# Kernel tuning notes

Measured on AMD Instinct MI355X. Metric: run time of the kernel, lower is better.

Reference implementation:

```python
import jax, jax.numpy as jnp
import numpy as np

NUM_HEADS = 16

def setup_inputs() -> dict:
    key = jax.random.key(0)
    k0, k1, k2, k3 = jax.random.split(key, 4)
    B, N, Nl, Nr, D = 16, 257, 514, 512, 1024
    gather_idx = jax.random.randint(k0, (B, N), 0, B * Nl + Nr, dtype=jnp.int64 if jax.config.jax_enable_x64 else jnp.int32)
    lhs_states = jax.random.normal(k1, (4, B, Nl, D), dtype=jnp.float32)
    rhs_states = jax.random.normal(k2, (4, 1, Nr, D), dtype=jnp.float32)
    Wo = jax.random.normal(k3, (D, D), dtype=jnp.float32) * 0.02
    bo = jnp.zeros((D,), dtype=jnp.float32)
    return {"gather_idx": gather_idx, "lhs_states": lhs_states, "rhs_states": rhs_states, "Wo": Wo, "bo": bo}


def _gather_stacked_batched_states(gather_idx, lhs_states, rhs_states):
    # lhs_states: [4, B, Nl, D] cache; rhs_states: [4, 1, Nr, D]
    # torch builds batched_states [4, 1, B*Nl+Nr, D] then gathers with [4, B, N, D] idx
    S, B, Nl, D = lhs_states.shape
    Nr = rhs_states.shape[2]
    batched = jnp.concatenate(
        [lhs_states.reshape(S, B * Nl, D), rhs_states.reshape(S, Nr, D)], axis=1
    )  # [4, B*Nl+Nr, D]
    N = gather_idx.shape[1]
    gathered = jnp.take(batched, gather_idx.reshape(-1), axis=1)  # [4, B*N, D]
    return gathered.reshape(S, B, N, D)


def reference(gather_idx, lhs_states, rhs_states, Wo, bo):
    # Gather hidden/q/k/v states from the expanded cache buffer (token reuse dispatch)
    gathered = _gather_stacked_batched_states(gather_idx, lhs_states, rhs_states)
    hidden, q, k, v = gathered[0], gathered[1], gathered[2], gathered[3]
    B, N, D = hidden.shape
    H = NUM_HEADS
    hd = D // H
    scale = hd ** -0.5
    # _shape: [B, N, D] -> [B, H, N, hd]; query scaled before bmm as in torch
    qh = (q * scale).reshape(B, N, H, hd).transpose(0, 2, 1, 3)
    kh = k.reshape(B, N, H, hd).transpose(0, 2, 1, 3)
    vh = v.reshape(B, N, H, hd).transpose(0, 2, 1, 3)
    attn_weights = jax.nn.softmax(jnp.einsum('bhqd,bhkd->bhqk', qh, kh), axis=-1)
    attn_out = jnp.einsum('bhqk,bhkd->bhqd', attn_weights, vh)  # [B, H, N, hd]
    attn_out = attn_out.transpose(0, 2, 1, 3).reshape(B, N, D)
    attn_out = attn_out @ Wo.T + bo  # out_proj (torch Linear)
    return hidden + attn_out  # residual
```

## Files before the change

### kernel.cpp

```cpp
#include <hip/hip_runtime.h>
#include <hip/hip_bf16.h>

typedef __attribute__((ext_vector_type(8))) short bf16x8;
typedef __attribute__((ext_vector_type(4))) float f32x4;
typedef unsigned short u16;
typedef unsigned int u32;

#define LHS_STRIDE 8421376
#define RHS_STRIDE 524288
#define TBL_SPLIT  8224
#define AN 257
#define KSD 68
#define VSD 260

__device__ __forceinline__ const float* tbl_row(int s, int g,
    const float* __restrict__ lhs, const float* __restrict__ rhs) {
  if (g < TBL_SPLIT) return lhs + (size_t)s * LHS_STRIDE + (size_t)g * 1024;
  return rhs + (size_t)s * RHS_STRIDE + (size_t)(g - TBL_SPLIT) * 1024;
}

__device__ __forceinline__ u16 f2b(float x) {
  union { __hip_bfloat16 b; u16 u; } c;
  c.b = __float2bfloat16(x);
  return c.u;
}

__device__ __forceinline__ u32 pk2(float a, float b) {
  return (u32)f2b(a) | ((u32)f2b(b) << 16);
}

__device__ __forceinline__ bf16x8 mk8(ushort4 a, ushort4 b) {
  bf16x8 r;
  r[0] = (short)a.x; r[1] = (short)a.y; r[2] = (short)a.z; r[3] = (short)a.w;
  r[4] = (short)b.x; r[5] = (short)b.y; r[6] = (short)b.z; r[7] = (short)b.w;
  return r;
}

__device__ __forceinline__ void gload16(const u16* g, u16* l) {
  __builtin_amdgcn_global_load_lds((const __attribute__((address_space(1))) void*)g,
                                   (__attribute__((address_space(3))) void*)l,
                                   16, 0, 0);
}

struct __align__(16) AttnSmem {
  u16 K[272 * KSD];
  u16 VT[64 * VSD];
};

__global__ __launch_bounds__(512, 2) void attn_kernel(
    const int* __restrict__ gidx, const float* __restrict__ lhs,
    const float* __restrict__ rhs, u16* __restrict__ attn_out,
    const float* __restrict__ Wo, u16* __restrict__ wo_bf) {
  __shared__ AttnSmem sm;
  const int bh = blockIdx.x, b = bh >> 4, h = bh & 15;
  const int t = threadIdx.x, wave = t >> 6, lane = t & 63;
  const int lg = lane >> 4, lr = lane & 15;
  const int* gi = gidx + b * AN;

  const int sr = t >> 4, c4v = (t & 15) * 4;
  float4 kreg[9], vreg[9];
#pragma unroll
  for (int p = 0; p < 9; ++p) {
    int r = p * 32 + sr;
    int rc = (r < AN) ? r : 0;
    int g = gi[rc];
    kreg[p] = *(const float4*)(tbl_row(2, g, lhs, rhs) + h * 64 + c4v);
    vreg[p] = *(const float4*)(tbl_row(3, g, lhs, rhs) + h * 64 + c4v);
  }

  const int ntile = (wave == 0) ? 3 : 2;
  const int rts[3] = {wave, wave + 8, 16};
  bf16x8 qa[3][2];
#pragma unroll
  for (int ti = 0; ti < 3; ++ti) {
    if (ti < ntile) {
      int qrow = rts[ti] * 16 + lr; if (qrow > 256) qrow = 256;
      int g = gi[qrow];
      const float* qp = tbl_row(1, g, lhs, rhs) + h * 64 + lg * 8;
#pragma unroll
      for (int kf = 0; kf < 2; ++kf) {
        float4 v0 = *(const float4*)(qp + kf * 32);
        float4 v1 = *(const float4*)(qp + kf * 32 + 4);
        bf16x8 a;
        a[0] = (short)f2b(0.125f * v0.x); a[1] = (short)f2b(0.125f * v0.y);
        a[2] = (short)f2b(0.125f * v0.z); a[3] = (short)f2b(0.125f * v0.w);
        a[4] = (short)f2b(0.125f * v1.x); a[5] = (short)f2b(0.125f * v1.y);
        a[6] = (short)f2b(0.125f * v1.z); a[7] = (short)f2b(0.125f * v1.w);
        qa[ti][kf] = a;
      }
    }
  }

  {
    const float4* src = (const float4*)Wo;
    ushort4* dst = (ushort4*)wo_bf;
    int i0 = bh * 1024 + t * 2;
#pragma unroll
    for (int u = 0; u < 2; ++u) {
      float4 v = src[i0 + u];
      dst[i0 + u] = make_ushort4(f2b(v.x), f2b(v.y), f2b(v.z), f2b(v.w));
    }
  }

#pragma unroll
  for (int p = 0; p < 9; ++p) {
    int r = p * 32 + sr;
    if (r < AN) {
      *(ushort4*)&sm.K[r * KSD + c4v] =
          make_ushort4(f2b(kreg[p].x), f2b(kreg[p].y), f2b(kreg[p].z), f2b(kreg[p].w));
      sm.VT[(c4v + 0) * VSD + r] = f2b(vreg[p].x);
      sm.VT[(c4v + 1) * VSD + r] = f2b(vreg[p].y);
      sm.VT[(c4v + 2) * VSD + r] = f2b(vreg[p].z);
      sm.VT[(c4v + 3) * VSD + r] = f2b(vreg[p].w);
    }
  }
  __syncthreads();

  const int srcE = lr + ((lane & 16) << 1);
  const int srcO = srcE + 16;
  const bool useE = (lg < 2);

  for (int ti = 0; ti < ntile; ++ti) {
    const int r0 = rts[ti] * 16;

    f32x4 s[17];
#pragma unroll
    for (int nf = 0; nf < 17; ++nf) {
      const u16* kp = &sm.K[(nf * 16 + lr) * KSD + lg * 8];
      ushort4 x0 = *(const ushort4*)kp;
      ushort4 x1 = *(const ushort4*)(kp + 4);
      ushort4 y0 = *(const ushort4*)(kp + 32);
      ushort4 y1 = *(const ushort4*)(kp + 36);
      f32x4 acc = {0.f, 0.f, 0.f, 0.f};
      acc = __builtin_amdgcn_mfma_f32_16x16x32_bf16(mk8(x0, x1), qa[ti][0], acc, 0, 0, 0);
      acc = __builtin_amdgcn_mfma_f32_16x16x32_bf16(mk8(y0, y1), qa[ti][1], acc, 0, 0, 0);
      s[nf] = acc;
    }
    s[16][1] = -1e30f; s[16][2] = -1e30f; s[16][3] = -1e30f;
    if (lg != 0) s[16][0] = -1e30f;

    float m = -1e30f;
#pragma unroll
    for (int nf = 0; nf < 17; ++nf)
      m = fmaxf(m, fmaxf(fmaxf(s[nf][0], s[nf][1]), fmaxf(s[nf][2], s[nf][3])));
    m = fmaxf(m, __shfl_xor(m, 16));
    m = fmaxf(m, __shfl_xor(m, 32));
    float sum = 0.f;
#pragma unroll
    for (int nf = 0; nf < 17; ++nf) {
#pragma unroll
      for (int r = 0; r < 4; ++r) {
        float w = __expf(s[nf][r] - m);
        s[nf][r] = w;
        sum += w;
      }
    }
    sum += __shfl_xor(sum, 16);
    sum += __shfl_xor(sum, 32);
    const float inv = 1.0f / sum;

    f32x4 zero = {0.f, 0.f, 0.f, 0.f};
    f32x4 o[4] = {zero, zero, zero, zero};
#pragma unroll
    for (int ks = 0; ks < 8; ++ks) {
      u32 e0 = pk2(s[2 * ks][0] * inv, s[2 * ks][1] * inv);
      u32 e1 = pk2(s[2 * ks][2] * inv, s[2 * ks][3] * inv);
      u32 f0 = pk2(s[2 * ks + 1][0] * inv, s[2 * ks + 1][1] * inv);
      u32 f1 = pk2(s[2 * ks + 1][2] * inv, s[2 * ks + 1][3] * inv);
      u32 A0 = (u32)__shfl((int)e0, srcE), A1 = (u32)__shfl((int)e1, srcE);
      u32 A2 = (u32)__shfl((int)e0, srcO), A3 = (u32)__shfl((int)e1, srcO);
      u32 B0 = (u32)__shfl((int)f0, srcE), B1 = (u32)__shfl((int)f1, srcE);
      u32 B2 = (u32)__shfl((int)f0, srcO), B3 = (u32)__shfl((int)f1, srcO);
      union { u32 w[4]; bf16x8 v; } pa;
      pa.w[0] = useE ? A0 : B0; pa.w[1] = useE ? A1 : B1;
      pa.w[2] = useE ? A2 : B2; pa.w[3] = useE ? A3 : B3;
#pragma unroll
      for (int nd = 0; nd < 4; ++nd) {
        const u16* vp = &sm.VT[(nd * 16 + lr) * VSD + ks * 32 + lg * 8];
        bf16x8 vb = mk8(*(const ushort4*)vp, *(const ushort4*)(vp + 4));
        o[nd] = __builtin_amdgcn_mfma_f32_16x16x32_bf16(pa.v, vb, o[nd], 0, 0, 0);
      }
    }
    {
      union { u32 w[4]; bf16x8 v; } pa;
      pa.w[0] = pk2(s[16][0] * inv, 0.f);
      pa.w[1] = 0; pa.w[2] = 0; pa.w[3] = 0;
#pragma unroll
      for (int nd = 0; nd < 4; ++nd) {
        union { u32 w[4]; bf16x8 v; } vb;
        vb.w[0] = (lg == 0) ? (u32)sm.VT[(nd * 16 + lr) * VSD + 256] : 0u;
        vb.w[1] = 0; vb.w[2] = 0; vb.w[3] = 0;
        o[nd] = __builtin_amdgcn_mfma_f32_16x16x32_bf16(pa.v, vb.v, o[nd], 0, 0, 0);
      }
    }

#pragma unroll
    for (int nd = 0; nd < 4; ++nd)
#pragma unroll
      for (int reg = 0; reg < 4; ++reg) {
        int row = r0 + lg * 4 + reg;
        if (row < AN)
          attn_out[(size_t)(b * AN + row) * 1024 + h * 64 + nd * 16 + lr] =
              f2b(o[nd][reg]);
      }
  }
}

__global__ __launch_bounds__(256, 1) void gemm_kernel(
    const u16* __restrict__ A, const u16* __restrict__ Bw,
    const float* __restrict__ bo, const int* __restrict__ gidx,
    const float* __restrict__ lhs, const float* __restrict__ rhs,
    float* __restrict__ out) {
  __shared__ __align__(16) u16 As[2][128 * 32];
  __shared__ __align__(16) u16 Bs[2][128 * 32];
  const int t = threadIdx.x, wave = t >> 6, lane = t & 63;
  const int lg = lane >> 4, lr = lane & 15;
  const int mt = blockIdx.x >> 3, nt = blockIdx.x & 7;
  const int m0 = mt * 128, n0 = nt * 128;
  const int wm = wave >> 1, wn = wave & 1;

  f32x4 zero = {0.f, 0.f, 0.f, 0.f};
  f32x4 acc[4][4];
#pragma unroll
  for (int i = 0; i < 4; ++i)
#pragma unroll
    for (int j = 0; j < 4; ++j) acc[i][j] = zero;

  const int srow = lane >> 2;
  const int scol = (((lane & 3) ^ ((lane >> 3) & 3))) * 8;
  const int ss = (lg ^ ((lr >> 1) & 3)) * 8;

#define STAGE(buf, kt)                                                          \
  {                                                                             \
    const int k0 = (kt) * 32;                                                   \
    _Pragma("unroll")                                                           \
    for (int i = 0; i < 2; ++i) {                                               \
      int row = wave * 32 + i * 16 + srow;                                      \
      int arow = m0 + row; if (arow > 4111) arow = 4111;                        \
      gload16(A + (size_t)arow * 1024 + k0 + scol, &As[buf][wave * 1024 + i * 512]); \
      gload16(Bw + (size_t)(n0 + row) * 1024 + k0 + scol, &Bs[buf][wave * 1024 + i * 512]); \
    }                                                                           \
  }

  STAGE(0, 0)
  __syncthreads();
  int cur = 0;
  for (int kt = 0; kt < 32; ++kt) {
    if (kt < 31) STAGE(cur ^ 1, kt + 1)
    bf16x8 af[4], bfr[4];
#pragma unroll
    for (int i = 0; i < 4; ++i) {
      af[i]  = *(const bf16x8*)&As[cur][(wm * 64 + i * 16 + lr) * 32 + ss];
      bfr[i] = *(const bf16x8*)&Bs[cur][(wn * 64 + i * 16 + lr) * 32 + ss];
    }
#pragma unroll
    for (int i = 0; i < 4; ++i)
#pragma unroll
      for (int j = 0; j < 4; ++j)
        acc[i][j] = __builtin_amdgcn_mfma_f32_16x16x32_bf16(af[i], bfr[j], acc[i][j], 0, 0, 0);
    __syncthreads();
    cur ^= 1;
  }
#undef STAGE

#pragma unroll
  for (int i = 0; i < 4; ++i)
#pragma unroll
    for (int j = 0; j < 4; ++j)
#pragma unroll
      for (int reg = 0; reg < 4; ++reg) {
        int row = m0 + wm * 64 + i * 16 + lg * 4 + reg;
        int col = n0 + wn * 64 + j * 16 + lr;
        if (row < 4112) {
          int g = gidx[row];
          out[(size_t)row * 1024 + col] =
              tbl_row(0, g, lhs, rhs)[col] + bo[col] + acc[i][j][reg];
        }
      }
}

extern "C" void kernel_launch(void* const* d_in, const int* in_sizes, int n_in,
                              void* d_out, int out_size, void* d_ws, size_t ws_size,
                              hipStream_t stream) {
  const int*   gidx = (const int*)d_in[0];
  const float* lhs  = (const float*)d_in[1];
  const float* rhs  = (const float*)d_in[2];
  const float* Wo   = (const float*)d_in[3];
  const float* bo   = (const float*)d_in[4];
  float* out = (float*)d_out;

  u16* attn_ws = (u16*)d_ws;
  u16* wo_bf   = attn_ws + (size_t)4112 * 1024;

  attn_kernel<<<256, 512, 0, stream>>>(gidx, lhs, rhs, attn_ws, Wo, wo_bf);
  gemm_kernel<<<264, 256, 0, stream>>>(attn_ws, wo_bf, bo, gidx, lhs, rhs, out);
}
```

Baseline: 302.2 us.

## Split gather and bf16 conversion into a separate full-row kernel before attention

Adds a gather_cvt kernel that fetches each gathered Q/K/V row and each Wo row as a full contiguous 4 KB fp32 row, converts it to bf16 and writes it to workspace. The attention kernel then reads compact bf16 tiles instead of doing scattered 256-byte fp32 gathers. The K smem stride also changes, and the GEMM block index is remapped so that concurrently scheduled blocks share A/B tiles differently. The cost is an extra launch and a round-trip of bf16 Q/K/V through global memory.

```diff
diff --git a/kernel.cpp b/kernel.cpp
--- a/kernel.cpp
+++ b/kernel.cpp
@@ -10,7 +10,8 @@
 #define RHS_STRIDE 524288
 #define TBL_SPLIT  8224
 #define AN 257
-#define KSD 68
+#define NR 4112
+#define KSD 72
 #define VSD 260
 
 __device__ __forceinline__ const float* tbl_row(int s, int g,
@@ -42,30 +43,64 @@
                                    16, 0, 0);
 }
 
+__global__ void gather_cvt_kernel(
+    const int* __restrict__ gidx, const float* __restrict__ lhs,
+    const float* __restrict__ rhs, const float* __restrict__ Wo,
+    u16* __restrict__ q_bf, u16* __restrict__ k_bf, u16* __restrict__ v_bf,
+    u16* __restrict__ wo_bf) {
+  const int blk = blockIdx.x, t = threadIdx.x;
+  const float* src;
+  u16* dst;
+  float sc = 1.0f;
+  if (blk < 3 * NR) {
+    const int s = blk / NR + 1;
+    const int row = blk - (s - 1) * NR;
+    src = tbl_row(s, gidx[row], lhs, rhs);
+    if (s == 1) { sc = 0.125f; dst = q_bf + (size_t)row * 1024; }
+    else if (s == 2) dst = k_bf + (size_t)row * 1024;
+    else dst = v_bf + (size_t)row * 1024;
+  } else {
+    const int row = blk - 3 * NR;
+    src = Wo + (size_t)row * 1024;
+    dst = wo_bf + (size_t)row * 1024;
+  }
+  float4 v = *(const float4*)(src + t * 4);
+  *(ushort4*)(dst + t * 4) =
+      make_ushort4(f2b(sc * v.x), f2b(sc * v.y), f2b(sc * v.z), f2b(sc * v.w));
+}
+
 struct __align__(16) AttnSmem {
   u16 K[272 * KSD];
   u16 VT[64 * VSD];
 };
 
-__global__ __launch_bounds__(512, 2) void attn_kernel(
-    const int* __restrict__ gidx, const float* __restrict__ lhs,
-    const float* __restrict__ rhs, u16* __restrict__ attn_out,
-    const float* __restrict__ Wo, u16* __restrict__ wo_bf) {
+__global__ __launch_bounds__(512) void attn_kernel(
+    const u16* __restrict__ q_bf, const u16* __restrict__ k_bf,
+    const u16* __restrict__ v_bf, u16* __restrict__ attn_out) {
   __shared__ AttnSmem sm;
   const int bh = blockIdx.x, b = bh >> 4, h = bh & 15;
   const int t = threadIdx.x, wave = t >> 6, lane = t & 63;
   const int lg = lane >> 4, lr = lane & 15;
-  const int* gi = gidx + b * AN;
-
-  const int sr = t >> 4, c4v = (t & 15) * 4;
-  float4 kreg[9], vreg[9];
-#pragma unroll
-  for (int p = 0; p < 9; ++p) {
-    int r = p * 32 + sr;
-    int rc = (r < AN) ? r : 0;
-    int g = gi[rc];
-    kreg[p] = *(const float4*)(tbl_row(2, g, lhs, rhs) + h * 64 + c4v);
-    vreg[p] = *(const float4*)(tbl_row(3, g, lhs, rhs) + h * 64 + c4v);
+  const u16* qb = q_bf + (size_t)b * AN * 1024 + h * 64;
+  const u16* kb = k_bf + (size_t)b * AN * 1024 + h * 64;
+  const u16* vb = v_bf + (size_t)b * AN * 1024 + h * 64;
+
+  {
+    const int r8 = t >> 3, c8 = (t & 7) * 8;
+#pragma unroll
+    for (int p = 0; p < 5; ++p) {
+      int r = p * 64 + r8;
+      if (r < AN) {
+        uint4 kx = *(const uint4*)(kb + (size_t)r * 1024 + c8);
+        *(uint4*)&sm.K[r * KSD + c8] = kx;
+        ushort4 v0 = *(const ushort4*)(vb + (size_t)r * 1024 + c8);
+        ushort4 v1 = *(const ushort4*)(vb + (size_t)r * 1024 + c8 + 4);
+        sm.VT[(c8 + 0) * VSD + r] = v0.x; sm.VT[(c8 + 1) * VSD + r] = v0.y;
+        sm.VT[(c8 + 2) * VSD + r] = v0.z; sm.VT[(c8 + 3) * VSD + r] = v0.w;
+        sm.VT[(c8 + 4) * VSD + r] = v1.x; sm.VT[(c8 + 5) * VSD + r] = v1.y;
+        sm.VT[(c8 + 6) * VSD + r] = v1.z; sm.VT[(c8 + 7) * VSD + r] = v1.w;
+      }
+    }
   }
 
   const int ntile = (wave == 0) ? 3 : 2;
@@ -75,43 +110,9 @@
   for (int ti = 0; ti < 3; ++ti) {
     if (ti < ntile) {
       int qrow = rts[ti] * 16 + lr; if (qrow > 256) qrow = 256;
-      int g = gi[qrow];
-      const float* qp = tbl_row(1, g, lhs, rhs) + h * 64 + lg * 8;
-#pragma unroll
-      for (int kf = 0; kf < 2; ++kf) {
-        float4 v0 = *(const float4*)(qp + kf * 32);
-        float4 v1 = *(const float4*)(qp + kf * 32 + 4);
-        bf16x8 a;
-        a[0] = (short)f2b(0.125f * v0.x); a[1] = (short)f2b(0.125f * v0.y);
-        a[2] = (short)f2b(0.125f * v0.z); a[3] = (short)f2b(0.125f * v0.w);
-        a[4] = (short)f2b(0.125f * v1.x); a[5] = (short)f2b(0.125f * v1.y);
-        a[6] = (short)f2b(0.125f * v1.z); a[7] = (short)f2b(0.125f * v1.w);
-        qa[ti][kf] = a;
-      }
-    }
-  }
-
-  {
-    const float4* src = (const float4*)Wo;
-    ushort4* dst = (ushort4*)wo_bf;
-    int i0 = bh * 1024 + t * 2;
-#pragma unroll
-    for (int u = 0; u < 2; ++u) {
-      float4 v = src[i0 + u];
-      dst[i0 + u] = make_ushort4(f2b(v.x), f2b(v.y), f2b(v.z), f2b(v.w));
-    }
-  }
-
-#pragma unroll
-  for (int p = 0; p < 9; ++p) {
-    int r = p * 32 + sr;
-    if (r < AN) {
-      *(ushort4*)&sm.K[r * KSD + c4v] =
-          make_ushort4(f2b(kreg[p].x), f2b(kreg[p].y), f2b(kreg[p].z), f2b(kreg[p].w));
-      sm.VT[(c4v + 0) * VSD + r] = f2b(vreg[p].x);
-      sm.VT[(c4v + 1) * VSD + r] = f2b(vreg[p].y);
-      sm.VT[(c4v + 2) * VSD + r] = f2b(vreg[p].z);
-      sm.VT[(c4v + 3) * VSD + r] = f2b(vreg[p].w);
+      const u16* qp = qb + (size_t)qrow * 1024 + lg * 8;
+      qa[ti][0] = *(const bf16x8*)qp;
+      qa[ti][1] = *(const bf16x8*)(qp + 32);
     }
   }
   __syncthreads();
@@ -177,8 +178,8 @@
 #pragma unroll
       for (int nd = 0; nd < 4; ++nd) {
         const u16* vp = &sm.VT[(nd * 16 + lr) * VSD + ks * 32 + lg * 8];
-        bf16x8 vb = mk8(*(const ushort4*)vp, *(const ushort4*)(vp + 4));
-        o[nd] = __builtin_amdgcn_mfma_f32_16x16x32_bf16(pa.v, vb, o[nd], 0, 0, 0);
+        bf16x8 vbr = mk8(*(const ushort4*)vp, *(const ushort4*)(vp + 4));
+        o[nd] = __builtin_amdgcn_mfma_f32_16x16x32_bf16(pa.v, vbr, o[nd], 0, 0, 0);
       }
     }
     {
@@ -187,10 +188,10 @@
       pa.w[1] = 0; pa.w[2] = 0; pa.w[3] = 0;
 #pragma unroll
       for (int nd = 0; nd < 4; ++nd) {
-        union { u32 w[4]; bf16x8 v; } vb;
-        vb.w[0] = (lg == 0) ? (u32)sm.VT[(nd * 16 + lr) * VSD + 256] : 0u;
-        vb.w[1] = 0; vb.w[2] = 0; vb.w[3] = 0;
-        o[nd] = __builtin_amdgcn_mfma_f32_16x16x32_bf16(pa.v, vb.v, o[nd], 0, 0, 0);
+        union { u32 w[4]; bf16x8 v; } vv;
+        vv.w[0] = (lg == 0) ? (u32)sm.VT[(nd * 16 + lr) * VSD + 256] : 0u;
+        vv.w[1] = 0; vv.w[2] = 0; vv.w[3] = 0;
+        o[nd] = __builtin_amdgcn_mfma_f32_16x16x32_bf16(pa.v, vv.v, o[nd], 0, 0, 0);
       }
     }
 
@@ -215,7 +216,8 @@
   __shared__ __align__(16) u16 Bs[2][128 * 32];
   const int t = threadIdx.x, wave = t >> 6, lane = t & 63;
   const int lg = lane >> 4, lr = lane & 15;
-  const int mt = blockIdx.x >> 3, nt = blockIdx.x & 7;
+  const int linear = (blockIdx.x & 7) * 33 + (blockIdx.x >> 3);
+  const int mt = linear >> 3, nt = linear & 7;
   const int m0 = mt * 128, n0 = nt * 128;
   const int wm = wave >> 1, wn = wave & 1;
 
@@ -289,9 +291,14 @@
   const float* bo   = (const float*)d_in[4];
   float* out = (float*)d_out;
 
-  u16* attn_ws = (u16*)d_ws;
-  u16* wo_bf   = attn_ws + (size_t)4112 * 1024;
-
-  attn_kernel<<<256, 512, 0, stream>>>(gidx, lhs, rhs, attn_ws, Wo, wo_bf);
+  u16* q_bf    = (u16*)d_ws;
+  u16* k_bf    = q_bf + (size_t)NR * 1024;
+  u16* v_bf    = k_bf + (size_t)NR * 1024;
+  u16* attn_ws = v_bf + (size_t)NR * 1024;
+  u16* wo_bf   = attn_ws + (size_t)NR * 1024;
+
+  gather_cvt_kernel<<<3 * NR + 1024, 256, 0, stream>>>(gidx, lhs, rhs, Wo,
+                                                       q_bf, k_bf, v_bf, wo_bf);
+  attn_kernel<<<256, 512, 0, stream>>>(q_bf, k_bf, v_bf, attn_ws);
   gemm_kernel<<<264, 256, 0, stream>>>(attn_ws, wo_bf, bo, gidx, lhs, rhs, out);
 }
```

Result: slower. 316.4 us (+4.7%).
